# Optimization experiments

Measured on AMD Instinct MI355X. Metric: run time of the kernel, lower is better.

Reference implementation:

```python
import jax, jax.numpy as jnp
import numpy as np

N = 4            # polynomial points per segment
SEGMENTS = 32
LENGTH = 2.0
HALF = 0.5 * LENGTH
IN_CH = 32
OUT_CH = 32
BATCH = 16
NODES = 1024


def _cheb_points(n):
    # Chebyshev-Lobatto points on [-1, 1] (LagrangePoly basis nodes)
    return -np.cos(np.pi * np.arange(n) / (n - 1))


def setup_inputs() -> dict:
    key = jax.random.key(0)
    k1, k2 = jax.random.split(key)
    x = jax.random.normal(k1, (BATCH, IN_CH, NODES), dtype=jnp.float32)
    # w.data.uniform_(-weight_magnitude, weight_magnitude)
    w = jax.random.uniform(k2, (OUT_CH, IN_CH, (N - 1) * SEGMENTS + 1),
                           dtype=jnp.float32, minval=-1.0, maxval=1.0)
    return {"x": x, "w": w}


def _lagrange_basis(x_in):
    # x_in: [b, c, m] -> basis values [b, c, m, n]
    X = jnp.asarray(_cheb_points(N), dtype=x_in.dtype)
    cols = []
    for j in range(N):
        b = jnp.ones_like(x_in)
        for m in range(N):
            if m != j:
                b = b * (x_in - X[m]) / (X[j] - X[m])
        cols.append(b)
    return jnp.stack(cols, axis=-1)


def reference(x, w):
    # bin index per element, clamped to valid segments
    id_min = jnp.clip(((x + HALF) / LENGTH * SEGMENTS).astype(jnp.int32), 0, SEGMENTS - 1)
    id_max = id_min + 1
    wid_min = id_min * (N - 1)                         # [b, c, m]
    idx = wid_min[..., None] + jnp.arange(N)           # [b, c, m, n]
    c_idx = jnp.arange(IN_CH)[None, :, None, None]     # broadcast channel index
    wg = w[:, c_idx, idx]                              # [o, b, c, m, n] irregular gather
    wg = jnp.transpose(wg, (1, 0, 2, 3, 4))            # [b, o, c, m, n]
    # map x into the local segment coordinate in [-half, half]
    x_min = id_min.astype(x.dtype) / SEGMENTS * 2.0 - 1.0
    x_max = id_max.astype(x.dtype) / SEGMENTS * 2.0 - 1.0
    x_in = LENGTH * (x - x_min) / (x_max - x_min) - HALF
    basis = _lagrange_basis(x_in)                      # [b, c, m, n]
    # sum over in_channels and polynomial points -> [b, o, m]
    return jnp.einsum('bcmj,bocmj->bom', basis, wg)
```

## Files before the change

kernel.cpp:

```cpp
#include <hip/hip_runtime.h>

#define NB 16
#define NC 32
#define NO 32
#define NM 1024
#define SEGS 32
#define WLEN 97
#define MT 8

__global__ __launch_bounds__(256) void repack_w_kernel(const float* __restrict__ w,
                                                       float4* __restrict__ w3) {
    int i = blockIdx.x * blockDim.x + threadIdx.x;
    if (i >= NC * SEGS * NO) return;
    int o   = i & 31;
    int seg = (i >> 5) & 31;
    int c   = i >> 10;
    const float* p = w + (o * NC + c) * WLEN + 3 * seg;
    w3[i] = make_float4(p[0], p[1], p[2], p[3]);
}

__device__ __forceinline__ float4 lagrange_basis(float xv, int& id_out) {
    float v  = (xv + 1.0f) * 16.0f;
    int   id = (int)v;
    id = min(max(id, 0), SEGS - 1);
    const float x_min = (float)id * 0.0625f - 1.0f;
    const float t     = (xv - x_min) * 32.0f - 1.0f;
    const float d0 = t + 1.0f;
    const float d1 = t + 0.5f;
    const float d2 = t - 0.5f;
    const float d3 = t - 1.0f;
    float4 bb;
    bb.x = d1 * d2 * d3 * (-0.66666667f);
    bb.y = d0 * d2 * d3 * ( 1.33333333f);
    bb.z = d0 * d1 * d3 * (-1.33333333f);
    bb.w = d0 * d1 * d2 * ( 0.66666667f);
    id_out = id;
    return bb;
}

__global__ __launch_bounds__(256) void pw_main_kernel(const float* __restrict__ x,
                                                      const float4* __restrict__ w3,
                                                      float* __restrict__ out) {
    const int blk = blockIdx.x;
    const int b   = blk >> 7;
    const int m0  = (blk & 127) * MT;

    __shared__ float4 sb[NC][MT];
    __shared__ int    soff[MT][36];

    const int tid = threadIdx.x;

    {
        const int c  = tid >> 3;
        const int mt = tid & 7;
        const float xv = x[(b * NC + c) * NM + m0 + mt];
        int id;
        float4 bb = lagrange_basis(xv, id);
        sb[c][mt]   = bb;
        soff[mt][c] = (c * SEGS + id) * NO;
    }
    __syncthreads();

    const int o  = tid & 31;
    const int mt = tid >> 5;

    int4 offs[8];
    {
        const int4* sp = (const int4*)&soff[mt][0];
#pragma unroll
        for (int k = 0; k < 8; ++k) offs[k] = sp[k];
    }

    const float4* __restrict__ wp = w3 + o;

    float acc = 0.0f;
#pragma unroll
    for (int k = 0; k < 8; ++k) {
        const int4 o4 = offs[k];
#pragma unroll
        for (int j = 0; j < 4; ++j) {
            const int c    = 4 * k + j;
            const int base = (j == 0) ? o4.x : (j == 1) ? o4.y : (j == 2) ? o4.z : o4.w;
            const float4 bb = sb[c][mt];
            const float4 wv = wp[base];
            acc = fmaf(bb.x, wv.x, acc);
            acc = fmaf(bb.y, wv.y, acc);
            acc = fmaf(bb.z, wv.z, acc);
            acc = fmaf(bb.w, wv.w, acc);
        }
    }

    out[(b * NO + o) * NM + m0 + mt] = acc;
}

__global__ __launch_bounds__(256) void pw_fallback_kernel(const float* __restrict__ x,
                                                          const float* __restrict__ w,
                                                          float* __restrict__ out) {
    const int blk = blockIdx.x;
    const int b   = blk >> 7;
    const int m   = (blk & 127) * 8 + (threadIdx.x & 7);
    const int o   = threadIdx.x >> 3;

    float acc = 0.0f;
    for (int c = 0; c < NC; ++c) {
        const float xv = x[(b * NC + c) * NM + m];
        int id;
        float4 bb = lagrange_basis(xv, id);
        const float* p = w + (o * NC + c) * WLEN + 3 * id;
        acc = fmaf(bb.x, p[0], acc);
        acc = fmaf(bb.y, p[1], acc);
        acc = fmaf(bb.z, p[2], acc);
        acc = fmaf(bb.w, p[3], acc);
    }
    out[(b * NO + o) * NM + m] = acc;
}

extern "C" void kernel_launch(void* const* d_in, const int* in_sizes, int n_in,
                              void* d_out, int out_size, void* d_ws, size_t ws_size,
                              hipStream_t stream) {
    const float* x = (const float*)d_in[0];
    const float* w = (const float*)d_in[1];
    float* out = (float*)d_out;

    const size_t w3_bytes = (size_t)NC * SEGS * NO * sizeof(float4);

    if (ws_size >= w3_bytes) {
        float4* w3 = (float4*)d_ws;
        repack_w_kernel<<<(NC * SEGS * NO + 255) / 256, 256, 0, stream>>>(w, w3);
        pw_main_kernel<<<NB * (NM / MT), 256, 0, stream>>>(x, w3, out);
    } else {
        pw_fallback_kernel<<<NB * (NM / 8), 256, 0, stream>>>(x, w, out);
    }
}
```

Baseline: 68.25 us.

## Stage bf16-packed weights in LDS and compute 64-point tiles per block

Repacks the weights as bf16 (8 bytes per 4-point segment instead of 16) and has each 1024-thread block copy half of the packed weight table (128 KB) into LDS, in two channel passes. The per-element weight gather then reads from LDS instead of global memory or cache. Each thread accumulates two m positions, and results are transposed through LDS so the output stores are coalesced float2 writes. In exchange, weight precision drops to bf16, occupancy falls to one large block per CU, and each block does a serial bulk load of 256 KB with no overlap against compute.

```diff
diff --git a/kernel.cpp b/kernel.cpp
--- a/kernel.cpp
+++ b/kernel.cpp
@@ -6,17 +6,31 @@
 #define NM 1024
 #define SEGS 32
 #define WLEN 97
-#define MT 8
+#define MTB 64
+
+#define WLDS_BYTES   131072
+#define BLDS_BYTES   16384
+#define SLDS_BYTES   4096
+#define SMEM_BYTES   (WLDS_BYTES + BLDS_BYTES + SLDS_BYTES)
+
+__device__ __forceinline__ unsigned f2bf(float f) {
+    unsigned u = __float_as_uint(f);
+    return (u + 0x7fffu + ((u >> 16) & 1u)) >> 16;
+}
 
 __global__ __launch_bounds__(256) void repack_w_kernel(const float* __restrict__ w,
-                                                       float4* __restrict__ w3) {
+                                                       uint2* __restrict__ w4) {
     int i = blockIdx.x * blockDim.x + threadIdx.x;
     if (i >= NC * SEGS * NO) return;
     int o   = i & 31;
     int seg = (i >> 5) & 31;
     int c   = i >> 10;
     const float* p = w + (o * NC + c) * WLEN + 3 * seg;
-    w3[i] = make_float4(p[0], p[1], p[2], p[3]);
+    unsigned b0 = f2bf(p[0]);
+    unsigned b1 = f2bf(p[1]);
+    unsigned b2 = f2bf(p[2]);
+    unsigned b3 = f2bf(p[3]);
+    w4[i] = make_uint2(b0 | (b1 << 16), b2 | (b3 << 16));
 }
 
 __device__ __forceinline__ float4 lagrange_basis(float xv, int& id_out) {
@@ -38,59 +52,93 @@
     return bb;
 }
 
-__global__ __launch_bounds__(256) void pw_main_kernel(const float* __restrict__ x,
-                                                      const float4* __restrict__ w3,
-                                                      float* __restrict__ out) {
+__global__ __launch_bounds__(1024, 4) void pw_main_kernel(const float* __restrict__ x,
+                                                          const uint2* __restrict__ w4,
+                                                          float* __restrict__ out) {
+    extern __shared__ char smem[];
+    uint2*  wlds = (uint2*)smem;
+    float4* blds = (float4*)(smem + WLDS_BYTES);
+    int*    slds = (int*)(smem + WLDS_BYTES + BLDS_BYTES);
+    float*  alds = (float*)(smem + WLDS_BYTES);
+
     const int blk = blockIdx.x;
-    const int b   = blk >> 7;
-    const int m0  = (blk & 127) * MT;
+    const int b   = blk >> 4;
+    const int m0  = (blk & 15) * MTB;
 
-    __shared__ float4 sb[NC][MT];
-    __shared__ int    soff[MT][36];
+    const int t     = threadIdx.x;
+    const int o     = t & 31;
+    const int mslot = t >> 5;
 
-    const int tid = threadIdx.x;
+    float acc0 = 0.0f, acc1 = 0.0f;
 
-    {
-        const int c  = tid >> 3;
-        const int mt = tid & 7;
-        const float xv = x[(b * NC + c) * NM + m0 + mt];
-        int id;
-        float4 bb = lagrange_basis(xv, id);
-        sb[c][mt]   = bb;
-        soff[mt][c] = (c * SEGS + id) * NO;
-    }
-    __syncthreads();
+#pragma unroll
+    for (int p = 0; p < 2; ++p) {
+        if (p) __syncthreads();
 
-    const int o  = tid & 31;
-    const int mt = tid >> 5;
+        {
+            const uint4* src = (const uint4*)(w4 + (size_t)p * 16 * SEGS * NO);
+            uint4* dst = (uint4*)wlds;
+#pragma unroll
+            for (int k = 0; k < 8; ++k) dst[t + 1024 * k] = src[t + 1024 * k];
+        }
 
-    int4 offs[8];
-    {
-        const int4* sp = (const int4*)&soff[mt][0];
+        {
+            const int cp = t >> 6;
+            const int m  = t & 63;
+            const float xv = x[(b * NC + p * 16 + cp) * NM + m0 + m];
+            int id;
+            float4 bb = lagrange_basis(xv, id);
+            blds[cp * 64 + m] = bb;
+            slds[m * 16 + cp] = ((cp * SEGS + id) * NO) * 8;
+        }
+        __syncthreads();
+
+        int4 offA[4], offB[4];
+        {
+            const int4* s0 = (const int4*)&slds[mslot * 16];
+            const int4* s1 = (const int4*)&slds[(mslot + 32) * 16];
 #pragma unroll
-        for (int k = 0; k < 8; ++k) offs[k] = sp[k];
-    }
+            for (int k = 0; k < 4; ++k) { offA[k] = s0[k]; offB[k] = s1[k]; }
+        }
 
-    const float4* __restrict__ wp = w3 + o;
-
-    float acc = 0.0f;
+        const char* wb = (const char*)wlds;
 #pragma unroll
-    for (int k = 0; k < 8; ++k) {
-        const int4 o4 = offs[k];
+        for (int k = 0; k < 4; ++k) {
+            const int4 oa = offA[k];
+            const int4 ob = offB[k];
 #pragma unroll
-        for (int j = 0; j < 4; ++j) {
-            const int c    = 4 * k + j;
-            const int base = (j == 0) ? o4.x : (j == 1) ? o4.y : (j == 2) ? o4.z : o4.w;
-            const float4 bb = sb[c][mt];
-            const float4 wv = wp[base];
-            acc = fmaf(bb.x, wv.x, acc);
-            acc = fmaf(bb.y, wv.y, acc);
-            acc = fmaf(bb.z, wv.z, acc);
-            acc = fmaf(bb.w, wv.w, acc);
+            for (int j = 0; j < 4; ++j) {
+                const int cp = 4 * k + j;
+                const int ba = (j == 0) ? oa.x : (j == 1) ? oa.y : (j == 2) ? oa.z : oa.w;
+                const int bbo = (j == 0) ? ob.x : (j == 1) ? ob.y : (j == 2) ? ob.z : ob.w;
+                const float4 B0 = blds[cp * 64 + mslot];
+                const float4 B1 = blds[cp * 64 + mslot + 32];
+                const uint2 pa = *(const uint2*)(wb + ba + o * 8);
+                const uint2 pb = *(const uint2*)(wb + bbo + o * 8);
+                acc0 = fmaf(B0.x, __uint_as_float(pa.x << 16), acc0);
+                acc0 = fmaf(B0.y, __uint_as_float(pa.x & 0xffff0000u), acc0);
+                acc0 = fmaf(B0.z, __uint_as_float(pa.y << 16), acc0);
+                acc0 = fmaf(B0.w, __uint_as_float(pa.y & 0xffff0000u), acc0);
+                acc1 = fmaf(B1.x, __uint_as_float(pb.x << 16), acc1);
+                acc1 = fmaf(B1.y, __uint_as_float(pb.x & 0xffff0000u), acc1);
+                acc1 = fmaf(B1.z, __uint_as_float(pb.y << 16), acc1);
+                acc1 = fmaf(B1.w, __uint_as_float(pb.y & 0xffff0000u), acc1);
+            }
         }
     }
 
-    out[(b * NO + o) * NM + m0 + mt] = acc;
+    __syncthreads();
+    alds[o * 66 + mslot]      = acc0;
+    alds[o * 66 + mslot + 32] = acc1;
+    __syncthreads();
+    {
+        const int o2 = t >> 5;
+        const int mw = t & 31;
+        float2 r;
+        r.x = alds[o2 * 66 + 2 * mw];
+        r.y = alds[o2 * 66 + 2 * mw + 1];
+        *(float2*)&out[(b * NO + o2) * NM + m0 + 2 * mw] = r;
+    }
 }
 
 __global__ __launch_bounds__(256) void pw_fallback_kernel(const float* __restrict__ x,
@@ -122,12 +170,18 @@
     const float* w = (const float*)d_in[1];
     float* out = (float*)d_out;
 
-    const size_t w3_bytes = (size_t)NC * SEGS * NO * sizeof(float4);
+    const size_t w4_bytes = (size_t)NC * SEGS * NO * sizeof(uint2);
 
-    if (ws_size >= w3_bytes) {
-        float4* w3 = (float4*)d_ws;
-        repack_w_kernel<<<(NC * SEGS * NO + 255) / 256, 256, 0, stream>>>(w, w3);
-        pw_main_kernel<<<NB * (NM / MT), 256, 0, stream>>>(x, w3, out);
+    static bool attr_set = false;
+    (void)attr_set;
+    hipError_t err = hipFuncSetAttribute((const void*)pw_main_kernel,
+                                         hipFuncAttributeMaxDynamicSharedMemorySize,
+                                         SMEM_BYTES);
+
+    if (err == hipSuccess && ws_size >= w4_bytes) {
+        uint2* w4 = (uint2*)d_ws;
+        repack_w_kernel<<<(NC * SEGS * NO + 255) / 256, 256, 0, stream>>>(w, w4);
+        pw_main_kernel<<<NB * (NM / MTB), 1024, SMEM_BYTES, stream>>>(x, w4, out);
     } else {
         pw_fallback_kernel<<<NB * (NM / 8), 256, 0, stream>>>(x, w, out);
     }
```

After: 64.66 us. 1.06x faster.
